# Kernel tuning notes

Hardware: AMD Instinct MI355X
Metric: run time of the kernel (lower is better)

## Reference

```python
import jax, jax.numpy as jnp
import numpy as np


def setup_inputs() -> dict:
    key = jax.random.key(0)
    ks = jax.random.split(key, 7)
    T, B, D, H, Q = 256, 128, 1024, 2048, 1024
    return {
        "x": jax.random.normal(ks[0], (T, B, D), dtype=jnp.float32),
        "h0": jax.random.normal(ks[1], (B, H), dtype=jnp.float32) * 0.01,
        "W_xh": jax.random.normal(ks[2], (D, H), dtype=jnp.float32) * 0.01,
        "W_hh": jax.random.normal(ks[3], (H, H), dtype=jnp.float32) * 0.01,
        "b_h": jnp.zeros((H,), dtype=jnp.float32),
        "W_hq": jax.random.normal(ks[4], (H, Q), dtype=jnp.float32) * 0.01,
        "b_q": jnp.zeros((Q,), dtype=jnp.float32),
    }


def reference(x, h0, W_xh, W_hh, b_h, W_hq, b_q):
    # x: (T, B, D); vanilla RNN recurrence with ReLU, per-step output projection.
    def step(h, xt):
        h = jax.nn.relu(xt @ W_xh + h @ W_hh + b_h)  # (B, H)
        return h, h @ W_hq + b_q                      # (B, Q)

    h, outs = jax.lax.scan(step, h0, x)               # outs: (T, B, Q)
    out = outs.reshape(-1, outs.shape[-1])            # torch.cat along dim 0 -> (T*B, Q)
    return out, h
```

## Files before the change

kernel.cpp:

```cpp
#include <hip/hip_runtime.h>
#include <hip/hip_bf16.h>

typedef __bf16 bf16_t;
typedef bf16_t bf16x8 __attribute__((ext_vector_type(8)));
typedef bf16_t bf16x4 __attribute__((ext_vector_type(4)));
typedef float f32x4 __attribute__((ext_vector_type(4)));
typedef float f32x2 __attribute__((ext_vector_type(2)));

__device__ __forceinline__ void load_lds16(const bf16_t* g, bf16_t* l) {
  __builtin_amdgcn_global_load_lds(
      (const __attribute__((address_space(1))) unsigned int*)g,
      (__attribute__((address_space(3))) unsigned int*)l,
      16, 0, 0);
}

__global__ void conv_f32_bf16(const float* __restrict__ src,
                              bf16_t* __restrict__ dst, long n) {
  long i = ((long)blockIdx.x * blockDim.x + threadIdx.x) * 8;
  if (i + 7 >= n) return;
  float4 a = *(const float4*)(src + i);
  float4 b = *(const float4*)(src + i + 4);
  bf16x8 v;
  v[0] = (bf16_t)a.x; v[1] = (bf16_t)a.y; v[2] = (bf16_t)a.z; v[3] = (bf16_t)a.w;
  v[4] = (bf16_t)b.x; v[5] = (bf16_t)b.y; v[6] = (bf16_t)b.z; v[7] = (bf16_t)b.w;
  *(bf16x8*)(dst + i) = v;
}

__global__ void conv_bf16_f32(const bf16_t* __restrict__ src,
                              float* __restrict__ dst, long n) {
  long i = (long)blockIdx.x * blockDim.x + threadIdx.x;
  if (i >= n) return;
  dst[i] = (float)src[i];
}

__global__ void transpose_conv(const float* __restrict__ src,
                               bf16_t* __restrict__ dst, int Ksrc, int Nsrc) {
  __shared__ float tile[32][33];
  int n0 = blockIdx.x * 32, k0 = blockIdx.y * 32;
  int tx = threadIdx.x, ty = threadIdx.y;
#pragma unroll
  for (int i = 0; i < 32; i += 8)
    tile[ty + i][tx] = src[(long)(k0 + ty + i) * Nsrc + n0 + tx];
  __syncthreads();
#pragma unroll
  for (int i = 0; i < 32; i += 8)
    dst[(long)(n0 + ty + i) * Ksrc + k0 + tx] = (bf16_t)tile[tx][ty + i];
}

template <int STORE_MODE>
__global__ __launch_bounds__(256) void gemm_bt_128(
    const bf16_t* __restrict__ A, const bf16_t* __restrict__ Bt,
    const float* __restrict__ bias, void* __restrict__ Dout,
    int M, int N, int K) {
  __shared__ bf16_t As[128 * 32];
  __shared__ bf16_t Bs[128 * 32];
  const int tid = threadIdx.x;
  const int lane = tid & 63;
  const int w = tid >> 6;
  const int wr = w >> 1, wc = w & 1;
  const int m0 = blockIdx.y * 128, n0 = blockIdx.x * 128;

  f32x4 acc[4][4] = {};

  const int r0 = tid >> 2;
  const int kk = (tid & 3) * 8;
  const int fr = lane & 15;
  const int fk = (lane >> 4) * 8;

  for (int k0 = 0; k0 < K; k0 += 32) {
    load_lds16(A + (long)(m0 + r0) * K + k0 + kk, As + w * 512);
    load_lds16(A + (long)(m0 + 64 + r0) * K + k0 + kk, As + 2048 + w * 512);
    load_lds16(Bt + (long)(n0 + r0) * K + k0 + kk, Bs + w * 512);
    load_lds16(Bt + (long)(n0 + 64 + r0) * K + k0 + kk, Bs + 2048 + w * 512);
    asm volatile("s_waitcnt vmcnt(0)" ::: "memory");
    __syncthreads();

    bf16x8 af[4], bfx[4];
#pragma unroll
    for (int m = 0; m < 4; ++m)
      af[m] = *(const bf16x8*)&As[(wr * 64 + m * 16 + fr) * 32 + fk];
#pragma unroll
    for (int n = 0; n < 4; ++n)
      bfx[n] = *(const bf16x8*)&Bs[(wc * 64 + n * 16 + fr) * 32 + fk];
#pragma unroll
    for (int m = 0; m < 4; ++m)
#pragma unroll
      for (int n = 0; n < 4; ++n)
        acc[m][n] = __builtin_amdgcn_mfma_f32_16x16x32_bf16(af[m], bfx[n],
                                                            acc[m][n], 0, 0, 0);
    __syncthreads();
  }

  const int fq = lane >> 4;
#pragma unroll
  for (int m = 0; m < 4; ++m) {
#pragma unroll
    for (int n = 0; n < 4; ++n) {
      int col = n0 + wc * 64 + n * 16 + fr;
      float bv = bias[col];
#pragma unroll
      for (int r = 0; r < 4; ++r) {
        int row = m0 + wr * 64 + m * 16 + fq * 4 + r;
        float v = acc[m][n][r] + bv;
        if (STORE_MODE == 0)
          ((float*)Dout)[(long)row * N + col] = v;
        else
          ((bf16_t*)Dout)[(long)row * N + col] = (bf16_t)v;
      }
    }
  }
}

__global__ __launch_bounds__(256, 1) void rnn_persistent4(
    const bf16_t* __restrict__ h0,
    bf16_t* __restrict__ Hbuf,
    const bf16_t* __restrict__ WhhT,
    unsigned int* __restrict__ flags) {
  __shared__ bf16_t Wlds[65536];
  __shared__ float sred[4][32 * 36];

  const int tid = threadIdx.x, lane = tid & 63, w = tid >> 6;
  const int gid = blockIdx.x;
  const int g = (gid >> 1) & 3;
  const int i = ((gid & 1) << 5) | (gid >> 3);
  const int m0 = g * 32, n0 = i * 32;
  const int H = 2048;
  const long BH = 128L * 2048;
  const int kb = w * 512;
  const int fr = lane & 15, fg = lane >> 4;
  const int w64 = w * 64;

  {
    const int scol = tid >> 3;
    const int sk = (tid & 7) * 8;
    const bf16_t* gsrc = WhhT + (long)(n0 + scol) * H + sk;
#pragma unroll 4
    for (int j = 0; j < 32; ++j) {
      bf16x8 v = *(const bf16x8*)(gsrc + j * 64);
      int k8 = j * 8 + (tid & 7);
      *(bf16x8*)&Wlds[(k8 * 32 + scol) * 8] = v;
    }
  }
  __syncthreads();

  const int jj = tid * 4;
  const int zrow = jj >> 5, zcol = jj & 31;
  const long zoff = (long)(m0 + zrow) * H + n0 + zcol;
  const int sidx = zrow * 36 + zcol;

  unsigned int* myflag = flags + ((g * 64 + i) << 4);
  const unsigned int* pollflag = flags + ((g * 64 + w * 16 + (lane & 15)) << 4);

  for (int t = 0; t < 256; ++t) {
    const bf16_t* hp = (t == 0) ? h0 : Hbuf + (long)(t - 1) * BH;
    bf16_t* z = Hbuf + (long)t * BH;

    f32x2 zvr;
    {
      const bf16_t* zp = z + zoff;
      asm volatile("global_load_dwordx2 %0, %1, off sc0 sc1"
                   : "=v"(zvr)
                   : "v"(zp)
                   : "memory");
    }

    if (t > 0) {
      unsigned int v;
      do {
        v = __hip_atomic_load(pollflag, __ATOMIC_RELAXED,
                              __HIP_MEMORY_SCOPE_AGENT);
        if (__all(v >= (unsigned int)t)) break;
        __builtin_amdgcn_s_sleep(1);
      } while (true);
    }

    const bf16_t* Ab0 = hp + (long)(m0 + fr) * H + kb + fg * 8;
    const bf16_t* Ab1 = Ab0 + (long)16 * H;
    f32x4 a0, a1, a2, a3, a4, a5, a6, a7, a8, a9, a10, a11, a12, a13, a14, a15;
    f32x4 c0, c1, c2, c3, c4, c5, c6, c7, c8, c9, c10, c11, c12, c13, c14, c15;
#define ABLOB(base)                                                           \
  "global_load_dwordx4 %0, %16, off sc0\n\t"                                  \
  "global_load_dwordx4 %1, %16, off offset:64 sc0\n\t"                        \
  "global_load_dwordx4 %2, %16, off offset:128 sc0\n\t"                       \
  "global_load_dwordx4 %3, %16, off offset:192 sc0\n\t"                       \
  "global_load_dwordx4 %4, %16, off offset:256 sc0\n\t"                       \
  "global_load_dwordx4 %5, %16, off offset:320 sc0\n\t"                       \
  "global_load_dwordx4 %6, %16, off offset:384 sc0\n\t"                       \
  "global_load_dwordx4 %7, %16, off offset:448 sc0\n\t"                       \
  "global_load_dwordx4 %8, %16, off offset:512 sc0\n\t"                       \
  "global_load_dwordx4 %9, %16, off offset:576 sc0\n\t"                       \
  "global_load_dwordx4 %10, %16, off offset:640 sc0\n\t"                      \
  "global_load_dwordx4 %11, %16, off offset:704 sc0\n\t"                      \
  "global_load_dwordx4 %12, %16, off offset:768 sc0\n\t"                      \
  "global_load_dwordx4 %13, %16, off offset:832 sc0\n\t"                      \
  "global_load_dwordx4 %14, %16, off offset:896 sc0\n\t"                      \
  "global_load_dwordx4 %15, %16, off offset:960 sc0"
    asm volatile(ABLOB(Ab0)
                 : "=&v"(a0), "=&v"(a1), "=&v"(a2), "=&v"(a3), "=&v"(a4),
                   "=&v"(a5), "=&v"(a6), "=&v"(a7), "=&v"(a8), "=&v"(a9),
                   "=&v"(a10), "=&v"(a11), "=&v"(a12), "=&v"(a13), "=&v"(a14),
                   "=&v"(a15)
                 : "v"(Ab0)
                 : "memory");
    asm volatile(ABLOB(Ab1)
                 : "=&v"(c0), "=&v"(c1), "=&v"(c2), "=&v"(c3), "=&v"(c4),
                   "=&v"(c5), "=&v"(c6), "=&v"(c7), "=&v"(c8), "=&v"(c9),
                   "=&v"(c10), "=&v"(c11), "=&v"(c12), "=&v"(c13), "=&v"(c14),
                   "=&v"(c15)
                 : "v"(Ab1)
                 : "memory");
#undef ABLOB

    f32x4 acc00 = {}, acc01 = {}, acc10 = {}, acc11 = {};
#define STEPX(ks, A, ACC0, ACC1)                                              \
  {                                                                           \
    bf16x8 w0 = *(const bf16x8*)&Wlds[((w64 + (ks) * 4 + fg) * 32 + fr) * 8]; \
    bf16x8 w1 =                                                               \
        *(const bf16x8*)&Wlds[((w64 + (ks) * 4 + fg) * 32 + 16 + fr) * 8];    \
    bf16x8 av = __builtin_bit_cast(bf16x8, A);                                \
    ACC0 = __builtin_amdgcn_mfma_f32_16x16x32_bf16(av, w0, ACC0, 0, 0, 0);    \
    ACC1 = __builtin_amdgcn_mfma_f32_16x16x32_bf16(av, w1, ACC1, 0, 0, 0);    \
  }
    asm volatile("s_waitcnt vmcnt(16)" ::: "memory");
    __builtin_amdgcn_sched_barrier(0);
    STEPX(0, a0, acc00, acc01)   STEPX(1, a1, acc00, acc01)
    STEPX(2, a2, acc00, acc01)   STEPX(3, a3, acc00, acc01)
    STEPX(4, a4, acc00, acc01)   STEPX(5, a5, acc00, acc01)
    STEPX(6, a6, acc00, acc01)   STEPX(7, a7, acc00, acc01)
    STEPX(8, a8, acc00, acc01)   STEPX(9, a9, acc00, acc01)
    STEPX(10, a10, acc00, acc01) STEPX(11, a11, acc00, acc01)
    STEPX(12, a12, acc00, acc01) STEPX(13, a13, acc00, acc01)
    STEPX(14, a14, acc00, acc01) STEPX(15, a15, acc00, acc01)
    asm volatile("s_waitcnt vmcnt(0)" ::: "memory");
    __builtin_amdgcn_sched_barrier(0);
    STEPX(0, c0, acc10, acc11)   STEPX(1, c1, acc10, acc11)
    STEPX(2, c2, acc10, acc11)   STEPX(3, c3, acc10, acc11)
    STEPX(4, c4, acc10, acc11)   STEPX(5, c5, acc10, acc11)
    STEPX(6, c6, acc10, acc11)   STEPX(7, c7, acc10, acc11)
    STEPX(8, c8, acc10, acc11)   STEPX(9, c9, acc10, acc11)
    STEPX(10, c10, acc10, acc11) STEPX(11, c11, acc10, acc11)
    STEPX(12, c12, acc10, acc11) STEPX(13, c13, acc10, acc11)
    STEPX(14, c14, acc10, acc11) STEPX(15, c15, acc10, acc11)
#undef STEPX

#pragma unroll
    for (int rr = 0; rr < 4; ++rr) {
      sred[w][(fg * 4 + rr) * 36 + fr] = acc00[rr];
      sred[w][(fg * 4 + rr) * 36 + 16 + fr] = acc01[rr];
      sred[w][(16 + fg * 4 + rr) * 36 + fr] = acc10[rr];
      sred[w][(16 + fg * 4 + rr) * 36 + 16 + fr] = acc11[rr];
    }
    __syncthreads();

    f32x4 r = *(const f32x4*)&sred[0][sidx];
    {
      f32x4 r1 = *(const f32x4*)&sred[1][sidx];
      f32x4 r2 = *(const f32x4*)&sred[2][sidx];
      f32x4 r3 = *(const f32x4*)&sred[3][sidx];
      r = r + r1 + r2 + r3;
    }
    bf16x4 zv = __builtin_bit_cast(bf16x4, zvr);
    bf16x4 o;
#pragma unroll
    for (int c4 = 0; c4 < 4; ++c4) {
      float v = r[c4] + (float)zv[c4];
      o[c4] = (bf16_t)(v > 0.f ? v : 0.f);
    }
    {
      f32x2 ov = __builtin_bit_cast(f32x2, o);
      const bf16_t* zp = z + zoff;
      asm volatile("global_store_dwordx2 %0, %1, off sc0 sc1" ::"v"(zp),
                   "v"(ov)
                   : "memory");
    }
    asm volatile("s_waitcnt vmcnt(0)" ::: "memory");
    __syncthreads();
    if (tid == 0)
      __hip_atomic_store(myflag, (unsigned int)(t + 1), __ATOMIC_RELAXED,
                         __HIP_MEMORY_SCOPE_AGENT);
  }
}

extern "C" void kernel_launch(void* const* d_in, const int* in_sizes, int n_in,
                              void* d_out, int out_size, void* d_ws,
                              size_t ws_size, hipStream_t stream) {
  const float* x   = (const float*)d_in[0];
  const float* h0  = (const float*)d_in[1];
  const float* Wxh = (const float*)d_in[2];
  const float* Whh = (const float*)d_in[3];
  const float* bh  = (const float*)d_in[4];
  const float* Whq = (const float*)d_in[5];
  const float* bq  = (const float*)d_in[6];
  float* out = (float*)d_out;

  const int T = 256, B = 128, D = 1024, H = 2048, Q = 1024;
  const long MB = (long)T * B;

  char* ws = (char*)d_ws;
  unsigned int* flags = (unsigned int*)ws;  ws += 256 * 64;
  bf16_t* x_bf = (bf16_t*)ws;  ws += MB * D * 2;
  bf16_t* Hbuf = (bf16_t*)ws;  ws += MB * H * 2;
  bf16_t* h0bf = (bf16_t*)ws;  ws += (long)B * H * 2;
  bf16_t* WxhT = (bf16_t*)ws;  ws += (long)H * D * 2;
  bf16_t* WhhT = (bf16_t*)ws;  ws += (long)H * H * 2;
  bf16_t* WhqT = (bf16_t*)ws;  ws += (long)Q * H * 2;

  hipMemsetAsync(flags, 0, 256 * 64, stream);

  conv_f32_bf16<<<(int)(MB * D / 8 / 256), 256, 0, stream>>>(x, x_bf, MB * D);
  conv_f32_bf16<<<(int)((long)B * H / 8 / 256), 256, 0, stream>>>(h0, h0bf,
                                                                  (long)B * H);
  transpose_conv<<<dim3(H / 32, D / 32), dim3(32, 8), 0, stream>>>(Wxh, WxhT, D, H);
  transpose_conv<<<dim3(H / 32, H / 32), dim3(32, 8), 0, stream>>>(Whh, WhhT, H, H);
  transpose_conv<<<dim3(Q / 32, H / 32), dim3(32, 8), 0, stream>>>(Whq, WhqT, H, Q);

  gemm_bt_128<1><<<dim3(H / 128, MB / 128), 256, 0, stream>>>(
      x_bf, WxhT, bh, Hbuf, (int)MB, H, D);

  rnn_persistent4<<<256, 256, 0, stream>>>(h0bf, Hbuf, WhhT, flags);

  gemm_bt_128<0><<<dim3(Q / 128, MB / 128), 256, 0, stream>>>(
      Hbuf, WhqT, bq, out, (int)MB, Q, H);

  conv_bf16_f32<<<(int)((long)B * H / 256), 256, 0, stream>>>(
      Hbuf + (long)(T - 1) * B * H, out + MB * Q, (long)B * H);
}
```

Before: 1.895 ms.

## Retile persistent RNN blocks to 16x64 with half of W_hh streamed from global

Each persistent block now owns 16 batch rows and 64 hidden columns instead of 32x32. Half of the W_hh tile stays in LDS and the other half is reloaded from global/L2 every step, issued before the flag spin-wait so the fetch overlaps synchronization. This halves the per-step h reads on the critical path after the barrier and reduces how many flags each block polls (32 instead of 64). In exchange it adds repeated weight traffic each step and more register pressure.

Result: slower. 2.220 ms (+17.1%).

```diff
diff --git a/kernel.cpp b/kernel.cpp
--- a/kernel.cpp
+++ b/kernel.cpp
@@ -4,6 +4,7 @@
 typedef __bf16 bf16_t;
 typedef bf16_t bf16x8 __attribute__((ext_vector_type(8)));
 typedef bf16_t bf16x4 __attribute__((ext_vector_type(4)));
+typedef bf16_t bf16x2 __attribute__((ext_vector_type(2)));
 typedef float f32x4 __attribute__((ext_vector_type(4)));
 typedef float f32x2 __attribute__((ext_vector_type(2)));
 
@@ -111,19 +112,19 @@
   }
 }
 
-__global__ __launch_bounds__(256, 1) void rnn_persistent4(
+__global__ __launch_bounds__(256, 1) void rnn_persistent7(
     const bf16_t* __restrict__ h0,
     bf16_t* __restrict__ Hbuf,
     const bf16_t* __restrict__ WhhT,
     unsigned int* __restrict__ flags) {
   __shared__ bf16_t Wlds[65536];
-  __shared__ float sred[4][32 * 36];
+  __shared__ float sred[4][16 * 68];
 
   const int tid = threadIdx.x, lane = tid & 63, w = tid >> 6;
   const int gid = blockIdx.x;
-  const int g = (gid >> 1) & 3;
-  const int i = ((gid & 1) << 5) | (gid >> 3);
-  const int m0 = g * 32, n0 = i * 32;
+  const int g = gid & 7;
+  const int i = gid >> 3;
+  const int m0 = g * 16, n0 = i * 64;
   const int H = 2048;
   const long BH = 128L * 2048;
   const int kb = w * 512;
@@ -144,41 +145,23 @@
   __syncthreads();
 
   const int jj = tid * 4;
-  const int zrow = jj >> 5, zcol = jj & 31;
-  const long zoff = (long)(m0 + zrow) * H + n0 + zcol;
-  const int sidx = zrow * 36 + zcol;
-
-  unsigned int* myflag = flags + ((g * 64 + i) << 4);
-  const unsigned int* pollflag = flags + ((g * 64 + w * 16 + (lane & 15)) << 4);
+  const int zrow = jj >> 6, zcol = jj & 63;
+  const int sidx = zrow * 68 + zcol;
+
+  unsigned int* myflag = flags + ((g * 32 + i) << 4);
+  const unsigned int* pollflag = flags + ((g * 32 + (lane & 31)) << 4);
+
+  const bf16_t* Wg2 = WhhT + (long)(n0 + 32 + fr) * H + kb + fg * 8;
+  const bf16_t* Wg3 = Wg2 + (long)16 * H;
 
   for (int t = 0; t < 256; ++t) {
     const bf16_t* hp = (t == 0) ? h0 : Hbuf + (long)(t - 1) * BH;
     bf16_t* z = Hbuf + (long)t * BH;
-
-    f32x2 zvr;
-    {
-      const bf16_t* zp = z + zoff;
-      asm volatile("global_load_dwordx2 %0, %1, off sc0 sc1"
-                   : "=v"(zvr)
-                   : "v"(zp)
-                   : "memory");
-    }
-
-    if (t > 0) {
-      unsigned int v;
-      do {
-        v = __hip_atomic_load(pollflag, __ATOMIC_RELAXED,
-                              __HIP_MEMORY_SCOPE_AGENT);
-        if (__all(v >= (unsigned int)t)) break;
-        __builtin_amdgcn_s_sleep(1);
-      } while (true);
-    }
-
-    const bf16_t* Ab0 = hp + (long)(m0 + fr) * H + kb + fg * 8;
-    const bf16_t* Ab1 = Ab0 + (long)16 * H;
-    f32x4 a0, a1, a2, a3, a4, a5, a6, a7, a8, a9, a10, a11, a12, a13, a14, a15;
+    const long zoff = (long)(m0 + zrow) * H + n0 + zcol;
+
+    f32x4 b0, b1, b2, b3, b4, b5, b6, b7, b8, b9, b10, b11, b12, b13, b14, b15;
     f32x4 c0, c1, c2, c3, c4, c5, c6, c7, c8, c9, c10, c11, c12, c13, c14, c15;
-#define ABLOB(base)                                                           \
+#define WBLOB                                                                 \
   "global_load_dwordx4 %0, %16, off sc0\n\t"                                  \
   "global_load_dwordx4 %1, %16, off offset:64 sc0\n\t"                        \
   "global_load_dwordx4 %2, %16, off offset:128 sc0\n\t"                       \
@@ -195,60 +178,96 @@
   "global_load_dwordx4 %13, %16, off offset:832 sc0\n\t"                      \
   "global_load_dwordx4 %14, %16, off offset:896 sc0\n\t"                      \
   "global_load_dwordx4 %15, %16, off offset:960 sc0"
-    asm volatile(ABLOB(Ab0)
-                 : "=&v"(a0), "=&v"(a1), "=&v"(a2), "=&v"(a3), "=&v"(a4),
-                   "=&v"(a5), "=&v"(a6), "=&v"(a7), "=&v"(a8), "=&v"(a9),
-                   "=&v"(a10), "=&v"(a11), "=&v"(a12), "=&v"(a13), "=&v"(a14),
-                   "=&v"(a15)
-                 : "v"(Ab0)
+    asm volatile(WBLOB
+                 : "=&v"(b0), "=&v"(b1), "=&v"(b2), "=&v"(b3), "=&v"(b4),
+                   "=&v"(b5), "=&v"(b6), "=&v"(b7), "=&v"(b8), "=&v"(b9),
+                   "=&v"(b10), "=&v"(b11), "=&v"(b12), "=&v"(b13), "=&v"(b14),
+                   "=&v"(b15)
+                 : "v"(Wg2)
                  : "memory");
-    asm volatile(ABLOB(Ab1)
+    asm volatile(WBLOB
                  : "=&v"(c0), "=&v"(c1), "=&v"(c2), "=&v"(c3), "=&v"(c4),
                    "=&v"(c5), "=&v"(c6), "=&v"(c7), "=&v"(c8), "=&v"(c9),
                    "=&v"(c10), "=&v"(c11), "=&v"(c12), "=&v"(c13), "=&v"(c14),
                    "=&v"(c15)
-                 : "v"(Ab1)
+                 : "v"(Wg3)
                  : "memory");
-#undef ABLOB
-
-    f32x4 acc00 = {}, acc01 = {}, acc10 = {}, acc11 = {};
-#define STEPX(ks, A, ACC0, ACC1)                                              \
+#undef WBLOB
+
+    f32x2 zvr;
+    {
+      const bf16_t* zp = z + zoff;
+      asm volatile("global_load_dwordx2 %0, %1, off sc0 sc1"
+                   : "=v"(zvr)
+                   : "v"(zp)
+                   : "memory");
+    }
+
+    if (t > 0) {
+      unsigned int v;
+      do {
+        v = __hip_atomic_load(pollflag, __ATOMIC_RELAXED,
+                              __HIP_MEMORY_SCOPE_AGENT);
+        if (__all(v >= (unsigned int)t)) break;
+        __builtin_amdgcn_s_sleep(1);
+      } while (true);
+    }
+
+    const bf16_t* Ab = hp + (long)(m0 + fr) * H + kb + fg * 8;
+    f32x4 a0, a1, a2, a3, a4, a5, a6, a7, a8, a9, a10, a11, a12, a13, a14, a15;
+    asm volatile(
+        "global_load_dwordx4 %0, %16, off sc0\n\t"
+        "global_load_dwordx4 %1, %16, off offset:64 sc0\n\t"
+        "global_load_dwordx4 %2, %16, off offset:128 sc0\n\t"
+        "global_load_dwordx4 %3, %16, off offset:192 sc0\n\t"
+        "global_load_dwordx4 %4, %16, off offset:256 sc0\n\t"
+        "global_load_dwordx4 %5, %16, off offset:320 sc0\n\t"
+        "global_load_dwordx4 %6, %16, off offset:384 sc0\n\t"
+        "global_load_dwordx4 %7, %16, off offset:448 sc0\n\t"
+        "global_load_dwordx4 %8, %16, off offset:512 sc0\n\t"
+        "global_load_dwordx4 %9, %16, off offset:576 sc0\n\t"
+        "global_load_dwordx4 %10, %16, off offset:640 sc0\n\t"
+        "global_load_dwordx4 %11, %16, off offset:704 sc0\n\t"
+        "global_load_dwordx4 %12, %16, off offset:768 sc0\n\t"
+        "global_load_dwordx4 %13, %16, off offset:832 sc0\n\t"
+        "global_load_dwordx4 %14, %16, off offset:896 sc0\n\t"
+        "global_load_dwordx4 %15, %16, off offset:960 sc0\n\t"
+        "s_waitcnt vmcnt(0)"
+        : "=&v"(a0), "=&v"(a1), "=&v"(a2), "=&v"(a3), "=&v"(a4), "=&v"(a5),
+          "=&v"(a6), "=&v"(a7), "=&v"(a8), "=&v"(a9), "=&v"(a10), "=&v"(a11),
+          "=&v"(a12), "=&v"(a13), "=&v"(a14), "=&v"(a15)
+        : "v"(Ab)
+        : "memory");
+    __builtin_amdgcn_sched_barrier(0);
+
+    f32x4 acc0 = {}, acc1 = {}, acc2 = {}, acc3 = {};
+#define STEPX(ks, A, B, C)                                                    \
   {                                                                           \
     bf16x8 w0 = *(const bf16x8*)&Wlds[((w64 + (ks) * 4 + fg) * 32 + fr) * 8]; \
     bf16x8 w1 =                                                               \
         *(const bf16x8*)&Wlds[((w64 + (ks) * 4 + fg) * 32 + 16 + fr) * 8];    \
     bf16x8 av = __builtin_bit_cast(bf16x8, A);                                \
-    ACC0 = __builtin_amdgcn_mfma_f32_16x16x32_bf16(av, w0, ACC0, 0, 0, 0);    \
-    ACC1 = __builtin_amdgcn_mfma_f32_16x16x32_bf16(av, w1, ACC1, 0, 0, 0);    \
-  }
-    asm volatile("s_waitcnt vmcnt(16)" ::: "memory");
-    __builtin_amdgcn_sched_barrier(0);
-    STEPX(0, a0, acc00, acc01)   STEPX(1, a1, acc00, acc01)
-    STEPX(2, a2, acc00, acc01)   STEPX(3, a3, acc00, acc01)
-    STEPX(4, a4, acc00, acc01)   STEPX(5, a5, acc00, acc01)
-    STEPX(6, a6, acc00, acc01)   STEPX(7, a7, acc00, acc01)
-    STEPX(8, a8, acc00, acc01)   STEPX(9, a9, acc00, acc01)
-    STEPX(10, a10, acc00, acc01) STEPX(11, a11, acc00, acc01)
-    STEPX(12, a12, acc00, acc01) STEPX(13, a13, acc00, acc01)
-    STEPX(14, a14, acc00, acc01) STEPX(15, a15, acc00, acc01)
-    asm volatile("s_waitcnt vmcnt(0)" ::: "memory");
-    __builtin_amdgcn_sched_barrier(0);
-    STEPX(0, c0, acc10, acc11)   STEPX(1, c1, acc10, acc11)
-    STEPX(2, c2, acc10, acc11)   STEPX(3, c3, acc10, acc11)
-    STEPX(4, c4, acc10, acc11)   STEPX(5, c5, acc10, acc11)
-    STEPX(6, c6, acc10, acc11)   STEPX(7, c7, acc10, acc11)
-    STEPX(8, c8, acc10, acc11)   STEPX(9, c9, acc10, acc11)
-    STEPX(10, c10, acc10, acc11) STEPX(11, c11, acc10, acc11)
-    STEPX(12, c12, acc10, acc11) STEPX(13, c13, acc10, acc11)
-    STEPX(14, c14, acc10, acc11) STEPX(15, c15, acc10, acc11)
+    bf16x8 g2 = __builtin_bit_cast(bf16x8, B);                                \
+    bf16x8 g3 = __builtin_bit_cast(bf16x8, C);                                \
+    acc0 = __builtin_amdgcn_mfma_f32_16x16x32_bf16(av, w0, acc0, 0, 0, 0);    \
+    acc1 = __builtin_amdgcn_mfma_f32_16x16x32_bf16(av, w1, acc1, 0, 0, 0);    \
+    acc2 = __builtin_amdgcn_mfma_f32_16x16x32_bf16(av, g2, acc2, 0, 0, 0);    \
+    acc3 = __builtin_amdgcn_mfma_f32_16x16x32_bf16(av, g3, acc3, 0, 0, 0);    \
+  }
+    STEPX(0, a0, b0, c0)    STEPX(1, a1, b1, c1)    STEPX(2, a2, b2, c2)
+    STEPX(3, a3, b3, c3)    STEPX(4, a4, b4, c4)    STEPX(5, a5, b5, c5)
+    STEPX(6, a6, b6, c6)    STEPX(7, a7, b7, c7)    STEPX(8, a8, b8, c8)
+    STEPX(9, a9, b9, c9)    STEPX(10, a10, b10, c10) STEPX(11, a11, b11, c11)
+    STEPX(12, a12, b12, c12) STEPX(13, a13, b13, c13) STEPX(14, a14, b14, c14)
+    STEPX(15, a15, b15, c15)
 #undef STEPX
 
 #pragma unroll
     for (int rr = 0; rr < 4; ++rr) {
-      sred[w][(fg * 4 + rr) * 36 + fr] = acc00[rr];
-      sred[w][(fg * 4 + rr) * 36 + 16 + fr] = acc01[rr];
-      sred[w][(16 + fg * 4 + rr) * 36 + fr] = acc10[rr];
-      sred[w][(16 + fg * 4 + rr) * 36 + 16 + fr] = acc11[rr];
+      sred[w][(fg * 4 + rr) * 68 + fr] = acc0[rr];
+      sred[w][(fg * 4 + rr) * 68 + 16 + fr] = acc1[rr];
+      sred[w][(fg * 4 + rr) * 68 + 32 + fr] = acc2[rr];
+      sred[w][(fg * 4 + rr) * 68 + 48 + fr] = acc3[rr];
     }
     __syncthreads();
 
@@ -317,7 +336,7 @@
   gemm_bt_128<1><<<dim3(H / 128, MB / 128), 256, 0, stream>>>(
       x_bf, WxhT, bh, Hbuf, (int)MB, H, D);
 
-  rnn_persistent4<<<256, 256, 0, stream>>>(h0bf, Hbuf, WhhT, flags);
+  rnn_persistent7<<<256, 256, 0, stream>>>(h0bf, Hbuf, WhhT, flags);
 
   gemm_bt_128<0><<<dim3(Q / 128, MB / 128), 256, 0, stream>>>(
       Hbuf, WhqT, bq, out, (int)MB, Q, H);
```
